# Kernel optimization log

Hardware: AMD Instinct MI355X
Metric: run time of the kernel (lower is better)

The kernel has to match this reference:

```python
import jax, jax.numpy as jnp
import numpy as np

N, E, IN_FT, OUT_FT = 8192, 4096, 512, 512
DENSITY = 0.02


def setup_inputs() -> dict:
    key = jax.random.key(0)
    k1, k2, k3, k4 = jax.random.split(key, 4)
    x = jax.random.normal(k1, (N, IN_FT), dtype=jnp.float32)
    hypergraph = (jax.random.uniform(k2, (N, E)) < DENSITY).astype(jnp.float32)
    # kaiming_uniform on [in, out]: fan_in = in_ft (torch fan of a Linear-style 2D param is dim 1 size? torch computes fan_in = size(1) for 2D -> out_ft here)
    bound_w = float(np.sqrt(6.0 / OUT_FT))  # kaiming_uniform a=sqrt(5)? default a=0 -> gain sqrt(2); bound = gain*sqrt(3/fan_in)
    bound_w = float(np.sqrt(2.0) * np.sqrt(3.0 / OUT_FT))
    weight = jax.random.uniform(k3, (IN_FT, OUT_FT), minval=-bound_w, maxval=bound_w, dtype=jnp.float32)
    bound_v = float(np.sqrt(2.0) * np.sqrt(3.0 / 1.0))
    V = jax.random.uniform(k4, (IN_FT, 1), minval=-bound_v, maxval=bound_v, dtype=jnp.float32)
    bias = jnp.zeros((OUT_FT,), dtype=jnp.float32)
    return {"x": x, "hypergraph": hypergraph, "weight": weight, "V": V, "bias": bias}


def reference(x, hypergraph, weight, V, bias):
    # edge embeddings: H^T @ x  -> [E, in_ft]
    edge_emb = hypergraph.T @ x
    hw = jax.nn.sigmoid(edge_emb @ V)          # [E, 1] learned hyperedge weights
    w = hw[:, 0]                                # [E]
    deg_v = (hypergraph @ hw)[:, 0]             # [N]  (sum over last dim of H @ hw)
    deg_e = jnp.sum(hypergraph, axis=0)         # [E]
    # adj = diag(deg_v) @ H @ diag(w) @ diag(deg_e) @ H^T @ diag(deg_v)
    # fused as broadcasted row/col scalings around two GEMMs (same math, no NxN)
    out = x @ weight                            # [N, out_ft]
    t = hypergraph.T @ (deg_v[:, None] * out)   # [E, out_ft]
    t = (w * deg_e)[:, None] * t                # diagonal edge scalings
    out = deg_v[:, None] * (hypergraph @ t)     # [N, out_ft]
    out = out + bias
    return (out, w)
```

## Files before the change

### kernel.cpp

```cpp
#include <hip/hip_runtime.h>


#define N_NODES 8192
#define N_EDGES 4096
#define FT 512

typedef short bf16x8 __attribute__((ext_vector_type(8)));
typedef float f32x4 __attribute__((ext_vector_type(4)));
typedef unsigned short u16;
typedef unsigned int u32;

__device__ __forceinline__ u16 f2b(float f) {
    union { float f; u32 u; } v; v.f = f;
    u32 r = v.u + 0x7FFFu + ((v.u >> 16) & 1u);
    return (u16)(r >> 16);
}
__device__ __forceinline__ float b2f(u16 h) {
    union { u32 u; float f; } v; v.u = ((u32)h) << 16; return v.f;
}


__global__ __launch_bounds__(256) void xv_xb_kernel(const float* __restrict__ x,
                                                    const float* __restrict__ V,
                                                    float* __restrict__ xv,
                                                    u16* __restrict__ xb,
                                                    float* __restrict__ zd) {
    if (blockIdx.x < 32) zd[blockIdx.x * 256 + threadIdx.x] = 0.f;
    int row = blockIdx.x * 4 + (threadIdx.x >> 6);
    int lane = threadIdx.x & 63;
    const float* xr = x + (size_t)row * FT + lane * 8;
    const float* vr = V + lane * 8;
    float4 a0 = *(const float4*)xr, a1 = *(const float4*)(xr + 4);
    float4 b0 = *(const float4*)vr, b1 = *(const float4*)(vr + 4);
    float acc = a0.x * b0.x + a0.y * b0.y + a0.z * b0.z + a0.w * b0.w +
                a1.x * b1.x + a1.y * b1.y + a1.z * b1.z + a1.w * b1.w;
    u16 tmp[8] = {f2b(a0.x), f2b(a0.y), f2b(a0.z), f2b(a0.w),
                  f2b(a1.x), f2b(a1.y), f2b(a1.z), f2b(a1.w)};
    *(uint4*)(xb + (size_t)row * FT + lane * 8) = *(uint4*)tmp;
#pragma unroll
    for (int off = 32; off; off >>= 1) acc += __shfl_down(acc, off);
    if (lane == 0) xv[row] = acc;
}

__global__ __launch_bounds__(256) void prep_h5_kernel(const float* __restrict__ H,
                                                      const float* __restrict__ xv,
                                                      u16* __restrict__ Hbf,
                                                      u16* __restrict__ HTbf,
                                                      float* __restrict__ zsum,
                                                      float* __restrict__ desum) {
    __shared__ u32 Wt[128][65];
    __shared__ float xvs[128];
    const int t = threadIdx.x;
    const int e0 = blockIdx.x * 128, n0 = blockIdx.y * 128;
    if (t < 128) xvs[t] = xv[n0 + t];
    const int r = t >> 1, h = t & 1;
    u32 o[32];
    {
        const float* src = H + (size_t)(n0 + r) * N_EDGES + e0 + h * 64;
#pragma unroll
        for (int j = 0; j < 16; j++) {
            float4 v = *(const float4*)(src + j * 4);
            o[2 * j]     = (v.x != 0.f ? 0x3F80u : 0u) | (v.y != 0.f ? 0x3F800000u : 0u);
            o[2 * j + 1] = (v.z != 0.f ? 0x3F80u : 0u) | (v.w != 0.f ? 0x3F800000u : 0u);
        }
#pragma unroll
        for (int k = 0; k < 32; k++) Wt[r][h * 32 + k] = o[k];
    }
    __syncthreads();
    {
        u16* hdst = Hbf + (size_t)(n0 + r) * N_EDGES + e0 + h * 64;
#pragma unroll
        for (int k = 0; k < 8; k++)
            *(uint4*)(hdst + k * 8) = *(uint4*)&o[k * 4];
    }
    {
        const int e = t >> 1, g = t & 1;
        const int ew = e >> 1;
        const u32 sel = (e & 1) ? 0x07060302u : 0x05040100u;
        u32 oo[32];
        float z = 0.f, d = 0.f;
#pragma unroll
        for (int j = 0; j < 32; j++) {
            int np = g * 32 + j;
            oo[j] = __builtin_amdgcn_perm(Wt[2 * np + 1][ew], Wt[2 * np][ew], sel);
            z += (oo[j] & 0xFFFFu) ? xvs[2 * np] : 0.f;
            d += (oo[j] & 0xFFFFu) ? 1.f : 0.f;
            z += (oo[j] >> 16) ? xvs[2 * np + 1] : 0.f;
            d += (oo[j] >> 16) ? 1.f : 0.f;
        }
        u16* drow = HTbf + (size_t)(e0 + e) * N_NODES + n0 + g * 64;
#pragma unroll
        for (int k = 0; k < 8; k++)
            *(uint4*)(drow + k * 8) = *(uint4*)&oo[k * 4];
        z += __shfl_down(z, 1);
        d += __shfl_down(d, 1);
        if (g == 0) {
            atomicAdd(zsum + e0 + e, z);
            atomicAdd(desum + e0 + e, d);
        }
    }
}

__global__ __launch_bounds__(256) void sigwt_kernel(const float* __restrict__ zsum,
                                                    const float* __restrict__ desum,
                                                    float* __restrict__ w_out,
                                                    float* __restrict__ wde,
                                                    const float* __restrict__ W,
                                                    u16* __restrict__ WT) {
    __shared__ float tile[32][33];
    int bx = blockIdx.x;
    if (bx < 16) {
        int e = bx * 256 + threadIdx.x;
        float z = zsum[e];
        float wv = 1.f / (1.f + expf(-z));
        w_out[e] = wv;
        wde[e] = wv * desum[e];
    } else {
        int b = bx - 16;
        int bxx = b & 15, byy = b >> 4;
        int tx = threadIdx.x & 31, ty = threadIdx.x >> 5;
        int c = bxx * 32 + tx;
        int r0 = byy * 32;
#pragma unroll
        for (int i = 0; i < 4; i++)
            tile[ty + i * 8][tx] = W[(size_t)(r0 + ty + i * 8) * FT + c];
        __syncthreads();
#pragma unroll
        for (int i = 0; i < 4; i++)
            WT[(size_t)(bxx * 32 + ty + i * 8) * FT + r0 + tx] = f2b(tile[tx][ty + i * 8]);
    }
}

__global__ __launch_bounds__(256) void degv_kernel(const u16* __restrict__ Hbf,
                                                   const float* __restrict__ w,
                                                   float* __restrict__ degv) {
    int row = blockIdx.x * 4 + (threadIdx.x >> 6);
    int lane = threadIdx.x & 63;
    const uint4* hr = (const uint4*)(Hbf + (size_t)row * N_EDGES);
    float acc = 0.f;
#pragma unroll
    for (int i = 0; i < 8; i++) {
        int idx = i * 64 + lane;
        uint4 h = hr[idx];
        const float* w8 = w + idx * 8;
        float4 wa = *(const float4*)w8, wb = *(const float4*)(w8 + 4);
        acc += (h.x & 0xFFFFu) ? wa.x : 0.f;  acc += (h.x >> 16) ? wa.y : 0.f;
        acc += (h.y & 0xFFFFu) ? wa.z : 0.f;  acc += (h.y >> 16) ? wa.w : 0.f;
        acc += (h.z & 0xFFFFu) ? wb.x : 0.f;  acc += (h.z >> 16) ? wb.y : 0.f;
        acc += (h.w & 0xFFFFu) ? wb.z : 0.f;  acc += (h.w >> 16) ? wb.w : 0.f;
    }
#pragma unroll
    for (int off = 32; off; off >>= 1) acc += __shfl_down(acc, off);
    if (lane == 0) degv[row] = acc;
}

__global__ void t2t_kernel(const u16* __restrict__ P, const float* __restrict__ wde,
                           u16* __restrict__ t2T) {
    __shared__ float tile[32][33];
    int tx = threadIdx.x, ty = threadIdx.y;
    int f0 = blockIdx.x * 32, e0 = blockIdx.y * 32;
#pragma unroll
    for (int i = 0; i < 4; i++) {
        int e = e0 + ty + i * 8;
        size_t idx = (size_t)e * 512 + f0 + tx;
        float s = 0.f;
#pragma unroll
        for (int sl = 0; sl < 8; sl++)
            s += b2f(P[idx + (size_t)sl * N_EDGES * 512]);
        tile[ty + i * 8][tx] = wde[e] * s;
    }
    __syncthreads();
#pragma unroll
    for (int i = 0; i < 4; i++)
        t2T[(size_t)(f0 + ty + i * 8) * N_EDGES + e0 + tx] = f2b(tile[tx][ty + i * 8]);
}

__global__ __launch_bounds__(256) void final_kernel(const u16* __restrict__ P,
                                                    const float* __restrict__ degv,
                                                    const float* __restrict__ bias,
                                                    float* __restrict__ out) {
    int i8 = blockIdx.x * 256 + threadIdx.x;
    int base = i8 * 8;
    int n = base >> 9, f = base & 511;
    float s[8] = {0.f, 0.f, 0.f, 0.f, 0.f, 0.f, 0.f, 0.f};
#pragma unroll
    for (int sl = 0; sl < 4; sl++) {
        uint4 v = *(const uint4*)(P + (size_t)sl * N_NODES * 512 + base);
        u32 ws[4] = {v.x, v.y, v.z, v.w};
#pragma unroll
        for (int j = 0; j < 4; j++) {
            s[2 * j]     += b2f((u16)(ws[j] & 0xFFFFu));
            s[2 * j + 1] += b2f((u16)(ws[j] >> 16));
        }
    }
    float dv = degv[n];
    float4 o0, o1;
    o0.x = dv * s[0] + bias[f + 0]; o0.y = dv * s[1] + bias[f + 1];
    o0.z = dv * s[2] + bias[f + 2]; o0.w = dv * s[3] + bias[f + 3];
    o1.x = dv * s[4] + bias[f + 4]; o1.y = dv * s[5] + bias[f + 5];
    o1.z = dv * s[6] + bias[f + 6]; o1.w = dv * s[7] + bias[f + 7];
    *(float4*)(out + base) = o0;
    *(float4*)(out + base + 4) = o1;
}


#define TBK 64

template <int MT, int NT, int EPI>
__global__ __launch_bounds__(256, 4)
void gemm9(const u16* __restrict__ Ap, const u16* __restrict__ Bp,
           void* __restrict__ Cp, const float* __restrict__ degv,
           int KC, int lda, int ldb, int ldc, size_t Ssz) {
    __shared__ __align__(16) u16 Alds[MT * 32 * TBK];
    __shared__ __align__(16) u16 Blds[NT * 32 * TBK];
    const int t = threadIdx.x;
    const int m0 = blockIdx.x * (MT * 32), n0 = blockIdx.y * (NT * 32);
    const int kbase = blockIdx.z * KC;
    const int wave = t >> 6, lane = t & 63, quad = lane >> 4, lo = lane & 15;
    const int wm = (wave >> 1) * (MT * 16), wn = (wave & 1) * (NT * 16);

    f32x4 acc[MT][NT];
#pragma unroll
    for (int a = 0; a < MT; a++)
#pragma unroll
        for (int b = 0; b < NT; b++) acc[a][b] = (f32x4){0.f, 0.f, 0.f, 0.f};

    for (int kk = 0; kk < KC; kk += TBK) {
        const int k0 = kbase + kk;
        __syncthreads();
#pragma unroll
        for (int i = 0; i < MT; i++) {
            int c = t + i * 256;
            int r = c >> 3;
            int j = ((c & 7) - r) & 7;
            const u16* g = Ap + (size_t)(m0 + r) * lda + k0 + j * 8;
            __builtin_amdgcn_global_load_lds((const u32*)g, (u32*)(Alds + c * 8), 16, 0, 0);
        }
#pragma unroll
        for (int i = 0; i < NT; i++) {
            int c = t + i * 256;
            int r = c >> 3;
            int j = ((c & 7) - r) & 7;
            const u16* g = Bp + (size_t)(n0 + r) * ldb + k0 + j * 8;
            __builtin_amdgcn_global_load_lds((const u32*)g, (u32*)(Blds + c * 8), 16, 0, 0);
        }
        __syncthreads();

#pragma unroll
        for (int s2 = 0; s2 < 2; s2++) {
            bf16x8 af[MT], bfr[NT];
#pragma unroll
            for (int mt = 0; mt < MT; mt++) {
                int m = wm + mt * 16 + lo;
                int s = (s2 * 4 + quad + m) & 7;
                af[mt] = *(const bf16x8*)&Alds[m * TBK + s * 8];
            }
#pragma unroll
            for (int nt = 0; nt < NT; nt++) {
                int n = wn + nt * 16 + lo;
                int s = (s2 * 4 + quad + n) & 7;
                bfr[nt] = *(const bf16x8*)&Blds[n * TBK + s * 8];
            }
#pragma unroll
            for (int mt = 0; mt < MT; mt++)
#pragma unroll
                for (int nt = 0; nt < NT; nt++)
                    acc[mt][nt] = __builtin_amdgcn_mfma_f32_16x16x32_bf16(af[mt], bfr[nt], acc[mt][nt], 0, 0, 0);
        }
    }

    if (EPI == 0) {
        u16* C = (u16*)Cp + (size_t)blockIdx.z * Ssz;
#pragma unroll
        for (int mt = 0; mt < MT; mt++) {
            int rb = m0 + wm + mt * 16 + quad * 4;
#pragma unroll
            for (int i = 0; i < 4; i++)
#pragma unroll
                for (int nt = 0; nt < NT; nt++)
                    C[(size_t)(rb + i) * ldc + n0 + wn + nt * 16 + lo] = f2b(acc[mt][nt][i]);
        }
    } else {
        u16* C = (u16*)Cp;
        float dv[NT];
#pragma unroll
        for (int nt = 0; nt < NT; nt++) dv[nt] = degv[n0 + wn + nt * 16 + lo];
#pragma unroll
        for (int mt = 0; mt < MT; mt++) {
            int rb = m0 + wm + mt * 16 + quad * 4;
#pragma unroll
            for (int i = 0; i < 4; i++)
#pragma unroll
                for (int nt = 0; nt < NT; nt++)
                    C[(size_t)(rb + i) * ldc + n0 + wn + nt * 16 + lo] =
                        f2b(acc[mt][nt][i] * dv[nt]);
        }
    }
}


extern "C" void kernel_launch(void* const* d_in, const int* in_sizes, int n_in,
                              void* d_out, int out_size, void* d_ws, size_t ws_size,
                              hipStream_t stream) {
    const float* x    = (const float*)d_in[0];
    const float* H    = (const float*)d_in[1];
    const float* W    = (const float*)d_in[2];
    const float* V    = (const float*)d_in[3];
    const float* bias = (const float*)d_in[4];
    float* out  = (float*)d_out;
    float* wout = out + (size_t)N_NODES * FT;
    (void)in_sizes; (void)n_in; (void)out_size; (void)ws_size;

    char* wsb = (char*)d_ws;
    float* wsf   = (float*)d_ws;
    float* xv    = wsf;
    float* zsum  = wsf + 8192;
    float* desum = wsf + 12288;
    float* degv  = wsf + 16384;
    float* wde   = wsf + 24576;
    u16*   Hbf   = (u16*)(wsb + 114688);
    u16*   HTbf  = (u16*)(wsb + 67223552);
    u16*   WT    = (u16*)(wsb + 134332416);
    u16*   doutT = (u16*)(wsb + 134856704);
    u16*   t2T   = (u16*)(wsb + 143245312);
    u16*   xb    = (u16*)(wsb + 147439616);
    u16*   P     = (u16*)(wsb + 155828224);

    xv_xb_kernel<<<N_NODES / 4, 256, 0, stream>>>(x, V, xv, xb, zsum);
    prep_h5_kernel<<<dim3(N_EDGES / 128, N_NODES / 128), 256, 0, stream>>>(
        H, xv, Hbf, HTbf, zsum, desum);
    sigwt_kernel<<<16 + 256, 256, 0, stream>>>(zsum, desum, wout, wde, W, WT);
    degv_kernel<<<N_NODES / 4, 256, 0, stream>>>(Hbf, wout, degv);

    gemm9<2, 4, 1><<<dim3(FT / 64, N_NODES / 128, 1), 256, 0, stream>>>(
        WT, xb, doutT, degv, FT, FT, FT, N_NODES, 0);

    gemm9<4, 4, 0><<<dim3(N_EDGES / 128, FT / 128, 8), 256, 0, stream>>>(
        HTbf, doutT, P, nullptr, N_NODES / 8, N_NODES, N_NODES, 512, (size_t)N_EDGES * 512);

    t2t_kernel<<<dim3(FT / 32, N_EDGES / 32), dim3(32, 8), 0, stream>>>(P, wde, t2T);

    gemm9<4, 4, 0><<<dim3(N_NODES / 128, FT / 128, 4), 256, 0, stream>>>(
        Hbf, t2T, P, nullptr, N_EDGES / 4, N_EDGES, N_EDGES, 512, (size_t)N_NODES * 512);

    final_kernel<<<(N_NODES * FT / 8) / 256, 256, 0, stream>>>(P, degv, bias, out);
}
```

Measured before the change: 360.6 us.

## Split H conversion and transpose into separate streaming and transpose kernels

Replaces the fused prep kernel, which read fp32 H, wrote both bf16 H and its transpose, and reduced per-edge sums, with two kernels. A grid-stride conversion kernel streams fp32 H to bf16 H. A second kernel reads bf16 H in 512x32 tiles, transposes through LDS, and writes HT with wave-level reductions and fewer atomics. This adds an extra pass over the 64MB bf16 H but gives each kernel simpler, more coalesced access patterns and a different store layout for HT.

Result: no change. 367.4 us (+1.9%).

```diff
diff --git a/kernel.cpp b/kernel.cpp
--- a/kernel.cpp
+++ b/kernel.cpp
@@ -42,61 +42,77 @@
     if (lane == 0) xv[row] = acc;
 }
 
-__global__ __launch_bounds__(256) void prep_h5_kernel(const float* __restrict__ H,
-                                                      const float* __restrict__ xv,
-                                                      u16* __restrict__ Hbf,
-                                                      u16* __restrict__ HTbf,
-                                                      float* __restrict__ zsum,
-                                                      float* __restrict__ desum) {
-    __shared__ u32 Wt[128][65];
-    __shared__ float xvs[128];
+__global__ __launch_bounds__(256) void conv_kernel(const float* __restrict__ H,
+                                                   u16* __restrict__ Hbf) {
+    size_t stride = (size_t)gridDim.x * 256;
+    size_t total = (size_t)N_NODES * N_EDGES / 16;
+    for (size_t it = blockIdx.x * 256 + threadIdx.x; it < total; it += stride) {
+        size_t base = it * 16;
+        const float* src = H + base;
+        u32 o[8];
+#pragma unroll
+        for (int j = 0; j < 4; j++) {
+            float4 h = *(const float4*)(src + j * 4);
+            o[2 * j]     = (h.x != 0.f ? 0x3F80u : 0u) | (h.y != 0.f ? 0x3F800000u : 0u);
+            o[2 * j + 1] = (h.z != 0.f ? 0x3F80u : 0u) | (h.w != 0.f ? 0x3F800000u : 0u);
+        }
+        u16* dst = Hbf + base;
+        *(uint4*)dst       = *(uint4*)&o[0];
+        *(uint4*)(dst + 8) = *(uint4*)&o[4];
+    }
+}
+
+__global__ __launch_bounds__(256) void trans2_kernel(const u16* __restrict__ Hbf,
+                                                     const float* __restrict__ xv,
+                                                     u16* __restrict__ HTbf,
+                                                     float* __restrict__ zsum,
+                                                     float* __restrict__ desum) {
+    __shared__ u32 Lt[512][17];
+    __shared__ float xvs[512];
     const int t = threadIdx.x;
-    const int e0 = blockIdx.x * 128, n0 = blockIdx.y * 128;
-    if (t < 128) xvs[t] = xv[n0 + t];
-    const int r = t >> 1, h = t & 1;
-    u32 o[32];
+    const int e0 = blockIdx.x * 32, n0 = blockIdx.y * 512;
+    xvs[t] = xv[n0 + t];
+    xvs[t + 256] = xv[n0 + t + 256];
     {
-        const float* src = H + (size_t)(n0 + r) * N_EDGES + e0 + h * 64;
-#pragma unroll
-        for (int j = 0; j < 16; j++) {
-            float4 v = *(const float4*)(src + j * 4);
-            o[2 * j]     = (v.x != 0.f ? 0x3F80u : 0u) | (v.y != 0.f ? 0x3F800000u : 0u);
-            o[2 * j + 1] = (v.z != 0.f ? 0x3F80u : 0u) | (v.w != 0.f ? 0x3F800000u : 0u);
-        }
-#pragma unroll
-        for (int k = 0; k < 32; k++) Wt[r][h * 32 + k] = o[k];
+        const int rb = t >> 2, q = t & 3;
+#pragma unroll
+        for (int pass = 0; pass < 8; pass++) {
+            int r = pass * 64 + rb;
+            const u32* src = (const u32*)(Hbf + (size_t)(n0 + r) * N_EDGES + e0);
+            uint4 v = *(const uint4*)(src + q * 4);
+            *(uint4*)&Lt[r][q * 4] = v;
+        }
     }
     __syncthreads();
     {
-        u16* hdst = Hbf + (size_t)(n0 + r) * N_EDGES + e0 + h * 64;
-#pragma unroll
-        for (int k = 0; k < 8; k++)
-            *(uint4*)(hdst + k * 8) = *(uint4*)&o[k * 4];
-    }
-    {
-        const int e = t >> 1, g = t & 1;
-        const int ew = e >> 1;
-        const u32 sel = (e & 1) ? 0x07060302u : 0x05040100u;
-        u32 oo[32];
-        float z = 0.f, d = 0.f;
-#pragma unroll
-        for (int j = 0; j < 32; j++) {
-            int np = g * 32 + j;
-            oo[j] = __builtin_amdgcn_perm(Wt[2 * np + 1][ew], Wt[2 * np][ew], sel);
-            z += (oo[j] & 0xFFFFu) ? xvs[2 * np] : 0.f;
-            d += (oo[j] & 0xFFFFu) ? 1.f : 0.f;
-            z += (oo[j] >> 16) ? xvs[2 * np + 1] : 0.f;
-            d += (oo[j] >> 16) ? 1.f : 0.f;
-        }
-        u16* drow = HTbf + (size_t)(e0 + e) * N_NODES + n0 + g * 64;
-#pragma unroll
-        for (int k = 0; k < 8; k++)
-            *(uint4*)(drow + k * 8) = *(uint4*)&oo[k * 4];
-        z += __shfl_down(z, 1);
-        d += __shfl_down(d, 1);
-        if (g == 0) {
-            atomicAdd(zsum + e0 + e, z);
-            atomicAdd(desum + e0 + e, d);
+        const int wv = t >> 6, l = t & 63;
+#pragma unroll
+        for (int k = 0; k < 8; k++) {
+            int el = wv + k * 4;
+            int e = e0 + el;
+            int ewl = el >> 1;
+            u32 sel = (el & 1) ? 0x07060302u : 0x05040100u;
+            u32* drow = (u32*)(HTbf + (size_t)e * N_NODES + n0);
+            float z = 0.f, d = 0.f;
+#pragma unroll
+            for (int j = 0; j < 4; j++) {
+                int np = l + 64 * j;
+                u32 v = __builtin_amdgcn_perm(Lt[2 * np + 1][ewl], Lt[2 * np][ewl], sel);
+                drow[np] = v;
+                z += (v & 0xFFFFu) ? xvs[2 * np] : 0.f;
+                d += (v & 0xFFFFu) ? 1.f : 0.f;
+                z += (v >> 16) ? xvs[2 * np + 1] : 0.f;
+                d += (v >> 16) ? 1.f : 0.f;
+            }
+#pragma unroll
+            for (int off = 32; off; off >>= 1) {
+                z += __shfl_down(z, off);
+                d += __shfl_down(d, off);
+            }
+            if (l == 0) {
+                atomicAdd(zsum + e, z);
+                atomicAdd(desum + e, d);
+            }
         }
     }
 }
@@ -327,8 +343,9 @@
     u16*   P     = (u16*)(wsb + 155828224);
 
     xv_xb_kernel<<<N_NODES / 4, 256, 0, stream>>>(x, V, xv, xb, zsum);
-    prep_h5_kernel<<<dim3(N_EDGES / 128, N_NODES / 128), 256, 0, stream>>>(
-        H, xv, Hbf, HTbf, zsum, desum);
+    conv_kernel<<<2048, 256, 0, stream>>>(H, Hbf);
+    trans2_kernel<<<dim3(N_EDGES / 32, N_NODES / 512), 256, 0, stream>>>(
+        Hbf, xv, HTbf, zsum, desum);
     sigwt_kernel<<<16 + 256, 256, 0, stream>>>(zsum, desum, wout, wde, W, WT);
     degv_kernel<<<N_NODES / 4, 256, 0, stream>>>(Hbf, wout, degv);
 
```
